# Optimization experiments

Measured on AMD Instinct MI355X. Metric: run time of the kernel, lower is better.

## Reference

```python
import jax, jax.numpy as jnp
import numpy as np

N, C, H, W_SP, E = 32, 64, 128, 128, 512


def setup_inputs() -> dict:
    key = jax.random.key(0)
    k1, k2, k3 = jax.random.split(key, 3)
    images = jax.random.normal(k1, (N, C, H, W_SP), dtype=jnp.float32)
    atts = jax.random.normal(k2, (N, E), dtype=jnp.float32)
    # nn.Linear(E, C*C): weight [C*C, E], bias [C*C]
    W = jax.random.normal(k3, (C * C, E), dtype=jnp.float32) * (1.0 / np.sqrt(E))
    b = jnp.zeros((C * C,), dtype=jnp.float32)
    return {"images": images, "atts": atts, "W": W, "b": b}


def reference(images, atts, W, b):
    n, c, h, w = images.shape
    logits = atts @ W.T + b                      # [N, C*C]
    a = jax.nn.softmax(logits, axis=-1)          # softmax over flattened C*C (first softmax)
    a = a.reshape(n, c, c)
    a = jax.nn.softmax(a, axis=-1)               # second softmax over last C (redundant but faithful)
    # out[n,c,h,w] = sum_d a[n,c,d] * images[n,d,h,w]  (batched [C,C]x[C,HW] matmul)
    out = jnp.einsum('ncd,ndhw->nchw', a, images)
    return out
```

## Files before the change

kernel.cpp:

```cpp
#include <hip/hip_runtime.h>
#include <hip/hip_bf16.h>

#define NB   32
#define CC   64
#define HW   16384
#define EE   512
#define CC2  4096

using short8  = __attribute__((ext_vector_type(8))) short;
using f32x16  = __attribute__((ext_vector_type(16))) float;

__device__ __forceinline__ unsigned short f2bf(float x) {
    unsigned int u = __float_as_uint(x);
    u += 0x7FFFu + ((u >> 16) & 1u);
    return (unsigned short)(u >> 16);
}

__global__ __launch_bounds__(256) void logits_kernel(
    const float* __restrict__ atts, const float* __restrict__ W,
    const float* __restrict__ b, float* __restrict__ logits) {
    const int t  = threadIdx.x;
    const int j  = blockIdx.x * 4 + (t & 3);
    const int n  = (t >> 2) & 31;
    const int kh = t >> 7;
    const float* __restrict__ wrow = W + (size_t)j * EE + kh * 256;
    const float* __restrict__ arow = atts + (size_t)n * EE + kh * 256;
    float acc0 = 0.f, acc1 = 0.f;
    #pragma unroll 4
    for (int k = 0; k < 256; k += 8) {
        float4 w0 = *reinterpret_cast<const float4*>(wrow + k);
        float4 a0 = *reinterpret_cast<const float4*>(arow + k);
        float4 w1 = *reinterpret_cast<const float4*>(wrow + k + 4);
        float4 a1 = *reinterpret_cast<const float4*>(arow + k + 4);
        acc0 = fmaf(w0.x, a0.x, acc0); acc0 = fmaf(w0.y, a0.y, acc0);
        acc0 = fmaf(w0.z, a0.z, acc0); acc0 = fmaf(w0.w, a0.w, acc0);
        acc1 = fmaf(w1.x, a1.x, acc1); acc1 = fmaf(w1.y, a1.y, acc1);
        acc1 = fmaf(w1.z, a1.z, acc1); acc1 = fmaf(w1.w, a1.w, acc1);
    }
    __shared__ float part[256];
    part[t] = acc0 + acc1;
    __syncthreads();
    if (t < 128) {
        logits[(size_t)n * CC2 + j] = part[t] + part[t + 128] + b[j];
    }
}

__global__ __launch_bounds__(256) void softmax_kernel(
    const float* __restrict__ logits, unsigned short* __restrict__ a_bf) {
    const int n = blockIdx.x;
    const int t = threadIdx.x;
    __shared__ float s[CC2];
    __shared__ float wmax[4];
    __shared__ float wsum[4];

    const float* __restrict__ L = logits + (size_t)n * CC2;

    float lmax = -1e30f;
    for (int i = t; i < CC2; i += 256) {
        float v = L[i];
        s[i] = v;
        lmax = fmaxf(lmax, v);
    }
    #pragma unroll
    for (int off = 32; off > 0; off >>= 1) lmax = fmaxf(lmax, __shfl_xor(lmax, off));
    if ((t & 63) == 0) wmax[t >> 6] = lmax;
    __syncthreads();
    const float bmax = fmaxf(fmaxf(wmax[0], wmax[1]), fmaxf(wmax[2], wmax[3]));

    float lsum = 0.f;
    for (int i = t; i < CC2; i += 256) {
        float e = __expf(s[i] - bmax);
        s[i] = e;
        lsum += e;
    }
    #pragma unroll
    for (int off = 32; off > 0; off >>= 1) lsum += __shfl_xor(lsum, off);
    if ((t & 63) == 0) wsum[t >> 6] = lsum;
    __syncthreads();
    const float inv = 1.f / (wsum[0] + wsum[1] + wsum[2] + wsum[3]);

    for (int i = t; i < CC2; i += 256) s[i] *= inv;
    __syncthreads();

    const int c = t >> 2;
    const int q = t & 3;
    const float* __restrict__ row = s + c * CC + q * 16;
    float mx = -1e30f;
    #pragma unroll
    for (int i = 0; i < 16; ++i) mx = fmaxf(mx, row[i]);
    mx = fmaxf(mx, __shfl_xor(mx, 1));
    mx = fmaxf(mx, __shfl_xor(mx, 2));
    float sum = 0.f;
    #pragma unroll
    for (int i = 0; i < 16; ++i) sum += __expf(row[i] - mx);
    sum += __shfl_xor(sum, 1);
    sum += __shfl_xor(sum, 2);
    const float isum = 1.f / sum;

    union { uint4 u[2]; unsigned short h[16]; } pk;
    #pragma unroll
    for (int i = 0; i < 16; ++i) pk.h[i] = f2bf(__expf(row[i] - mx) * isum);
    uint4* __restrict__ dst =
        reinterpret_cast<uint4*>(a_bf + (size_t)n * CC2 + c * CC + q * 16);
    dst[0] = pk.u[0];
    dst[1] = pk.u[1];
}

__global__ __launch_bounds__(512) void einsum_kernel(
    const float* __restrict__ img, const unsigned short* __restrict__ a_bf,
    float* __restrict__ out) {
    const int t    = threadIdx.x;
    const int lane = t & 63;
    const int wv   = t >> 6;
    const int n    = blockIdx.y;
    const int px0  = blockIdx.x * 256;
    const int lh   = lane >> 5;
    const int lc   = lane & 31;

    __shared__ unsigned short sImg[CC * 256];

    {
        const int px_l = (t & 63) * 4;
        const int d0   = (t >> 6) * 8;
        const float* __restrict__ gp = img + (size_t)n * (CC * HW) + px0 + px_l;
        #pragma unroll
        for (int i = 0; i < 8; ++i) {
            const int d = d0 + i;
            const float4 v = *reinterpret_cast<const float4*>(gp + (size_t)d * HW);
            union { uint2 u; unsigned short h[4]; } pk;
            pk.h[0] = f2bf(v.x); pk.h[1] = f2bf(v.y);
            pk.h[2] = f2bf(v.z); pk.h[3] = f2bf(v.w);
            *reinterpret_cast<uint2*>(&sImg[d * 256 + px_l]) = pk.u;
        }
    }
    __syncthreads();

    const int px_w = wv * 32 + lc;
    const unsigned short* __restrict__ ap = a_bf + (size_t)n * CC2;

    f32x16 acc0 = {};
    f32x16 acc1 = {};

    #pragma unroll
    for (int ks = 0; ks < 4; ++ks) {
        const int kbase = ks * 16 + lh * 8;
        union { short8 v; unsigned short h[8]; } bf;
        #pragma unroll
        for (int e = 0; e < 8; ++e)
            bf.h[e] = sImg[(kbase + e) * 256 + px_w];
        short8 a0 = *reinterpret_cast<const short8*>(ap + (size_t)lc * CC + kbase);
        short8 a1 = *reinterpret_cast<const short8*>(ap + (size_t)(lc + 32) * CC + kbase);
        acc0 = __builtin_amdgcn_mfma_f32_32x32x16_bf16(a0, bf.v, acc0, 0, 0, 0);
        acc1 = __builtin_amdgcn_mfma_f32_32x32x16_bf16(a1, bf.v, acc1, 0, 0, 0);
    }

    float* __restrict__ op = out + (size_t)n * (CC * HW) + px0 + px_w;
    #pragma unroll
    for (int r = 0; r < 16; ++r) {
        const int row = (r & 3) + 8 * (r >> 2) + 4 * lh;
        op[(size_t)row * HW]        = acc0[r];
        op[(size_t)(row + 32) * HW] = acc1[r];
    }
}

extern "C" void kernel_launch(void* const* d_in, const int* in_sizes, int n_in,
                              void* d_out, int out_size, void* d_ws, size_t ws_size,
                              hipStream_t stream) {
    const float* images = (const float*)d_in[0];
    const float* atts   = (const float*)d_in[1];
    const float* W      = (const float*)d_in[2];
    const float* b      = (const float*)d_in[3];
    float* out = (float*)d_out;

    float* logits = (float*)d_ws;
    unsigned short* a_bf = (unsigned short*)(logits + NB * CC2);

    logits_kernel<<<CC2 / 4, 256, 0, stream>>>(atts, W, b, logits);
    softmax_kernel<<<NB, 256, 0, stream>>>(logits, a_bf);
    einsum_kernel<<<dim3(HW / 256, NB), 512, 0, stream>>>(images, a_bf, out);
}
```

Measured before the change: 101.1 us.

## Pre-pack attention matrix in MFMA layout, split logits K four ways, nontemporal output stores

The logits kernel now gives each block 2 output columns and splits K into four 128-wide chunks, which doubles the block count. The softmax kernel writes the bf16 attention matrix already laid out in MFMA A-operand fragment order, so einsum lanes load contiguous 16-byte chunks. The einsum kernel hoists all eight image loads ahead of the conversions, adds an occupancy hint to launch bounds, and writes output with nontemporal stores so the streaming result does not pollute cache. The einsum is memory-bound on image reads and output writes, so the gains are expected to be small and the extra launch-bound constraint could raise register pressure.

```diff
diff --git a/kernel.cpp b/kernel.cpp
--- a/kernel.cpp
+++ b/kernel.cpp
@@ -20,14 +20,14 @@
     const float* __restrict__ atts, const float* __restrict__ W,
     const float* __restrict__ b, float* __restrict__ logits) {
     const int t  = threadIdx.x;
-    const int j  = blockIdx.x * 4 + (t & 3);
-    const int n  = (t >> 2) & 31;
-    const int kh = t >> 7;
-    const float* __restrict__ wrow = W + (size_t)j * EE + kh * 256;
-    const float* __restrict__ arow = atts + (size_t)n * EE + kh * 256;
+    const int j  = blockIdx.x * 2 + (t & 1);
+    const int n  = (t >> 1) & 31;
+    const int kq = t >> 6;
+    const float* __restrict__ wrow = W + (size_t)j * EE + kq * 128;
+    const float* __restrict__ arow = atts + (size_t)n * EE + kq * 128;
     float acc0 = 0.f, acc1 = 0.f;
-    #pragma unroll 4
-    for (int k = 0; k < 256; k += 8) {
+    #pragma unroll
+    for (int k = 0; k < 128; k += 8) {
         float4 w0 = *reinterpret_cast<const float4*>(wrow + k);
         float4 a0 = *reinterpret_cast<const float4*>(arow + k);
         float4 w1 = *reinterpret_cast<const float4*>(wrow + k + 4);
@@ -40,13 +40,16 @@
     __shared__ float part[256];
     part[t] = acc0 + acc1;
     __syncthreads();
-    if (t < 128) {
-        logits[(size_t)n * CC2 + j] = part[t] + part[t + 128] + b[j];
+    if (t < 64) {
+        const int jj = blockIdx.x * 2 + (t & 1);
+        const int nn = t >> 1;
+        const float r = part[t] + part[t + 64] + part[t + 128] + part[t + 192];
+        logits[(size_t)nn * CC2 + jj] = r + b[jj];
     }
 }
 
 __global__ __launch_bounds__(256) void softmax_kernel(
-    const float* __restrict__ logits, unsigned short* __restrict__ a_bf) {
+    const float* __restrict__ logits, unsigned short* __restrict__ a_pk) {
     const int n = blockIdx.x;
     const int t = threadIdx.x;
     __shared__ float s[CC2];
@@ -100,14 +103,17 @@
     union { uint4 u[2]; unsigned short h[16]; } pk;
     #pragma unroll
     for (int i = 0; i < 16; ++i) pk.h[i] = f2bf(__expf(row[i] - mx) * isum);
-    uint4* __restrict__ dst =
-        reinterpret_cast<uint4*>(a_bf + (size_t)n * CC2 + c * CC + q * 16);
-    dst[0] = pk.u[0];
-    dst[1] = pk.u[1];
+
+    const int half = c >> 5;
+    const int lc2  = c & 31;
+    unsigned short* __restrict__ base =
+        a_pk + (size_t)n * CC2 + (size_t)(q * 2 + half) * 512;
+    *reinterpret_cast<uint4*>(base + lc2 * 8)        = pk.u[0];
+    *reinterpret_cast<uint4*>(base + (32 + lc2) * 8) = pk.u[1];
 }
 
-__global__ __launch_bounds__(512) void einsum_kernel(
-    const float* __restrict__ img, const unsigned short* __restrict__ a_bf,
+__global__ __launch_bounds__(512, 4) void einsum_kernel(
+    const float* __restrict__ img, const unsigned short* __restrict__ a_pk,
     float* __restrict__ out) {
     const int t    = threadIdx.x;
     const int lane = t & 63;
@@ -123,20 +129,27 @@
         const int px_l = (t & 63) * 4;
         const int d0   = (t >> 6) * 8;
         const float* __restrict__ gp = img + (size_t)n * (CC * HW) + px0 + px_l;
-        #pragma unroll
-        for (int i = 0; i < 8; ++i) {
-            const int d = d0 + i;
-            const float4 v = *reinterpret_cast<const float4*>(gp + (size_t)d * HW);
-            union { uint2 u; unsigned short h[4]; } pk;
-            pk.h[0] = f2bf(v.x); pk.h[1] = f2bf(v.y);
-            pk.h[2] = f2bf(v.z); pk.h[3] = f2bf(v.w);
-            *reinterpret_cast<uint2*>(&sImg[d * 256 + px_l]) = pk.u;
-        }
+        float4 v0 = *reinterpret_cast<const float4*>(gp + (size_t)(d0 + 0) * HW);
+        float4 v1 = *reinterpret_cast<const float4*>(gp + (size_t)(d0 + 1) * HW);
+        float4 v2 = *reinterpret_cast<const float4*>(gp + (size_t)(d0 + 2) * HW);
+        float4 v3 = *reinterpret_cast<const float4*>(gp + (size_t)(d0 + 3) * HW);
+        float4 v4 = *reinterpret_cast<const float4*>(gp + (size_t)(d0 + 4) * HW);
+        float4 v5 = *reinterpret_cast<const float4*>(gp + (size_t)(d0 + 5) * HW);
+        float4 v6 = *reinterpret_cast<const float4*>(gp + (size_t)(d0 + 6) * HW);
+        float4 v7 = *reinterpret_cast<const float4*>(gp + (size_t)(d0 + 7) * HW);
+        union { uint2 u; unsigned short h[4]; } pk;
+        #define STG(i, vv) \
+            pk.h[0] = f2bf(vv.x); pk.h[1] = f2bf(vv.y); \
+            pk.h[2] = f2bf(vv.z); pk.h[3] = f2bf(vv.w); \
+            *reinterpret_cast<uint2*>(&sImg[(d0 + i) * 256 + px_l]) = pk.u;
+        STG(0, v0) STG(1, v1) STG(2, v2) STG(3, v3)
+        STG(4, v4) STG(5, v5) STG(6, v6) STG(7, v7)
+        #undef STG
     }
     __syncthreads();
 
     const int px_w = wv * 32 + lc;
-    const unsigned short* __restrict__ ap = a_bf + (size_t)n * CC2;
+    const unsigned short* __restrict__ apn = a_pk + (size_t)n * CC2;
 
     f32x16 acc0 = {};
     f32x16 acc1 = {};
@@ -148,8 +161,8 @@
         #pragma unroll
         for (int e = 0; e < 8; ++e)
             bf.h[e] = sImg[(kbase + e) * 256 + px_w];
-        short8 a0 = *reinterpret_cast<const short8*>(ap + (size_t)lc * CC + kbase);
-        short8 a1 = *reinterpret_cast<const short8*>(ap + (size_t)(lc + 32) * CC + kbase);
+        short8 a0 = *reinterpret_cast<const short8*>(apn + (ks * 2 + 0) * 512 + lane * 8);
+        short8 a1 = *reinterpret_cast<const short8*>(apn + (ks * 2 + 1) * 512 + lane * 8);
         acc0 = __builtin_amdgcn_mfma_f32_32x32x16_bf16(a0, bf.v, acc0, 0, 0, 0);
         acc1 = __builtin_amdgcn_mfma_f32_32x32x16_bf16(a1, bf.v, acc1, 0, 0, 0);
     }
@@ -158,8 +171,8 @@
     #pragma unroll
     for (int r = 0; r < 16; ++r) {
         const int row = (r & 3) + 8 * (r >> 2) + 4 * lh;
-        op[(size_t)row * HW]        = acc0[r];
-        op[(size_t)(row + 32) * HW] = acc1[r];
+        __builtin_nontemporal_store(acc0[r], op + (size_t)row * HW);
+        __builtin_nontemporal_store(acc1[r], op + (size_t)(row + 32) * HW);
     }
 }
 
@@ -173,9 +186,9 @@
     float* out = (float*)d_out;
 
     float* logits = (float*)d_ws;
-    unsigned short* a_bf = (unsigned short*)(logits + NB * CC2);
+    unsigned short* a_pk = (unsigned short*)(logits + NB * CC2);
 
-    logits_kernel<<<CC2 / 4, 256, 0, stream>>>(atts, W, b, logits);
-    softmax_kernel<<<NB, 256, 0, stream>>>(logits, a_bf);
-    einsum_kernel<<<dim3(HW / 256, NB), 512, 0, stream>>>(images, a_bf, out);
+    logits_kernel<<<CC2 / 2, 256, 0, stream>>>(atts, W, b, logits);
+    softmax_kernel<<<NB, 256, 0, stream>>>(logits, a_pk);
+    einsum_kernel<<<dim3(HW / 256, NB), 512, 0, stream>>>(images, a_pk, out);
 }
```

Result: faster. 84.22 us (-16.7%).
